# Kernel optimization log

Hardware: AMD Instinct MI355X
Metric: run time of the kernel (lower is better)

The kernel has to match this reference:

```python
import jax, jax.numpy as jnp
import numpy as np


def _sobel_filters():
    # 3D Sobel kernels for x, y, z directions, shape (3, 1, 3, 3, 3) in OIDHW.
    x = np.array([[[-1, 0, 1], [-2, 0, 2], [-1, 0, 1]],
                  [[-2, 0, 2], [-4, 0, 4], [-2, 0, 2]],
                  [[-1, 0, 1], [-2, 0, 2], [-1, 0, 1]]], dtype=np.float32)
    y = np.array([[[1, 2, 1], [0, 0, 0], [-1, -2, -1]],
                  [[2, 4, 2], [0, 0, 0], [-2, -4, -2]],
                  [[1, 2, 1], [0, 0, 0], [-1, -2, -1]]], dtype=np.float32)
    z = np.array([[[1, 2, 1], [2, 4, 2], [1, 2, 1]],
                  [[0, 0, 0], [0, 0, 0], [0, 0, 0]],
                  [[-1, -2, -1], [-2, -4, -2], [-1, -2, -1]]], dtype=np.float32)
    return jnp.asarray(np.stack([x, y, z])[:, None])  # (3,1,3,3,3)


_FILTERS = _sobel_filters()
_EPS = 1e-10


def gradient3d(x):
    # x: [B,1,D,H,W] -> gradient magnitude [B,1,D,H,W].
    # Single conv with 3 output channels == three separate torch conv3d + concat.
    g = jax.lax.conv_general_dilated(
        x, _FILTERS, window_strides=(1, 1, 1),
        padding=[(1, 1), (1, 1), (1, 1)],
        dimension_numbers=('NCDHW', 'OIDHW', 'NCDHW'))  # [B,3,D,H,W]
    return jnp.sqrt(jnp.sum(g * g, axis=1, keepdims=True) + _EPS)


def setup_inputs() -> dict:
    key = jax.random.key(0)
    k1, k2, k3 = jax.random.split(key, 3)
    shape = (2, 1, 192, 192, 192)
    pred = jax.random.normal(k1, shape, dtype=jnp.float32)
    gt_dose = jax.random.normal(k2, shape, dtype=jnp.float32)
    body_mask = (jax.random.uniform(k3, shape) > 0.3).astype(jnp.float32)
    return {"pred": pred, "gt_dose": gt_dose, "body_mask": body_mask}


def reference(pred, gt_dose, body_mask):
    mse = jnp.square(pred - gt_dose) * body_mask
    mge = jnp.square(gradient3d(gt_dose) - gradient3d(pred)) * body_mask
    return jnp.mean(mse + jnp.tanh(mge) * mse)
```

## Files before the change

### kernel.cpp

```cpp
#include <hip/hip_runtime.h>
#include <math.h>

#define W 192
#define H 192
#define DEPTH 192
#define BATCH 2
#define TW 64
#define TH 8
#define DC 12
#define HW (H * W)
#define VOL ((size_t)DEPTH * HW)
#define LROW 72
#define LPLANE (LROW * 10)
#define NPAIR ((DC + 2) / 2)
#define NITEM 720

__global__ __launch_bounds__(256) void sobel_loss_part(
    const float* __restrict__ pred, const float* __restrict__ gt,
    const float* __restrict__ mask, float* __restrict__ partials)
{
    __shared__ __align__(16) float lds[2 * 2 * LPLANE];

    const int tid = threadIdx.x;
    const int tx = blockIdx.x % 3;
    const int ty = blockIdx.x / 3;
    const int w0 = tx * TW, h0 = ty * TH;
    const int d0 = blockIdx.y * DC;
    const size_t base = (size_t)blockIdx.z * VOL;

    const int wy  = tid >> 5;
    const int wxo = (tid & 31) << 1;
    const size_t moff = base + (size_t)(h0 + wy) * W + (w0 + wxo);

    int it_ok[3], it_st[3], it_q[3], it_lds[3];
    size_t it_goff[3];
    const float* it_src[3];
    #pragma unroll
    for (int k = 0; k < 3; ++k) {
        int j = tid + 256 * k;
        int jj = (j < NITEM) ? j : 0;
        int a = jj / 360; int pj = jj - a * 360;
        int q = pj / 180; int e = pj - q * 180;
        int r = e / 18;   int c = e - r * 18;
        int y  = h0 - 1 + r;
        int xf = w0 - 4 + 4 * c;
        it_st[k]  = (j < NITEM);
        it_ok[k]  = it_st[k] && ((unsigned)y < (unsigned)H) && ((unsigned)xf < (unsigned)W);
        it_goff[k] = it_ok[k] ? ((size_t)y * W + xf) : 0;
        it_lds[k]  = ((a * 2 + q) * 10 + r) * LROW + 4 * c;
        it_q[k]    = q;
        it_src[k]  = a ? gt : pred;
    }

    float4 R[3];
    auto load_pair = [&](int s) {
        const int p0 = d0 - 1 + 2 * s;
        #pragma unroll
        for (int k = 0; k < 3; ++k) {
            const int p = p0 + it_q[k];
            const bool v = it_ok[k] && (p >= 0) && (p < DEPTH);
            R[k] = v ? *(const float4*)(it_src[k] + base + (size_t)p * HW + it_goff[k])
                     : make_float4(0.f, 0.f, 0.f, 0.f);
        }
    };

    float2 Mn = make_float2(0.f, 0.f), Mn1 = make_float2(0.f, 0.f);
    float2 Mc, Mc1;
    auto load_mask = [&](int s) {
        Mn  = *(const float2*)(mask + moff + (size_t)(d0 + 2 * s - 2) * HW);
        Mn1 = *(const float2*)(mask + moff + (size_t)(d0 + 2 * s - 1) * HW);
    };

    float dx[2][2][3], dy[2][2][3], sm[2][2][3], ct[2][2][2];
    #pragma unroll
    for (int a = 0; a < 2; ++a)
        #pragma unroll
        for (int o = 0; o < 2; ++o) {
            dx[a][o][0]=dx[a][o][1]=dx[a][o][2]=0.f;
            dy[a][o][0]=dy[a][o][1]=dy[a][o][2]=0.f;
            sm[a][o][0]=sm[a][o][1]=sm[a][o][2]=0.f;
            ct[a][o][0]=ct[a][o][1]=0.f;
        }
    float acc = 0.f;

    load_pair(0);

    for (int s = 0; s < NPAIR; ++s) {
        __syncthreads();
        #pragma unroll
        for (int k = 0; k < 3; ++k)
            if (it_st[k]) *(float4*)(lds + it_lds[k]) = R[k];
        __syncthreads();

        Mc = Mn; Mc1 = Mn1;
        if (s + 1 < NPAIR) {
            load_pair(s + 1);
            load_mask(s + 1);
        }

        #pragma unroll
        for (int q = 0; q < 2; ++q) {
            const int p = d0 - 1 + 2 * s + q;
            float e[2][3][4];
            #pragma unroll
            for (int a = 0; a < 2; ++a)
                #pragma unroll
                for (int r = 0; r < 3; ++r)
                    #pragma unroll
                    for (int c = 0; c < 4; ++c)
                        e[a][r][c] = lds[(a * 2 + q) * LPLANE + (wy + r) * LROW + wxo + 3 + c];

            #pragma unroll
            for (int a = 0; a < 2; ++a)
                #pragma unroll
                for (int o = 0; o < 2; ++o) {
                    float s0 = e[a][0][o] + 2.f * e[a][0][o+1] + e[a][0][o+2];
                    float s1 = e[a][1][o] + 2.f * e[a][1][o+1] + e[a][1][o+2];
                    float s2 = e[a][2][o] + 2.f * e[a][2][o+1] + e[a][2][o+2];
                    float dd0 = e[a][0][o+2] - e[a][0][o];
                    float dd1 = e[a][1][o+2] - e[a][1][o];
                    float dd2 = e[a][2][o+2] - e[a][2][o];
                    dx[a][o][0] = dx[a][o][1]; dx[a][o][1] = dx[a][o][2]; dx[a][o][2] = dd0 + 2.f * dd1 + dd2;
                    sm[a][o][0] = sm[a][o][1]; sm[a][o][1] = sm[a][o][2]; sm[a][o][2] = s0 + 2.f * s1 + s2;
                    dy[a][o][0] = dy[a][o][1]; dy[a][o][1] = dy[a][o][2]; dy[a][o][2] = s0 - s2;
                    ct[a][o][0] = ct[a][o][1]; ct[a][o][1] = e[a][1][o+1];
                }

            if (p >= d0 + 1) {
                const float2 M = q ? Mc1 : Mc;
                #pragma unroll
                for (int o = 0; o < 2; ++o) {
                    float gxa = dx[0][o][0] + 2.f * dx[0][o][1] + dx[0][o][2];
                    float gya = dy[0][o][0] + 2.f * dy[0][o][1] + dy[0][o][2];
                    float gza = sm[0][o][0] - sm[0][o][2];
                    float gxb = dx[1][o][0] + 2.f * dx[1][o][1] + dx[1][o][2];
                    float gyb = dy[1][o][0] + 2.f * dy[1][o][1] + dy[1][o][2];
                    float gzb = sm[1][o][0] - sm[1][o][2];
                    float ga = __builtin_amdgcn_sqrtf(gxa * gxa + gya * gya + gza * gza + 1e-10f);
                    float gb = __builtin_amdgcn_sqrtf(gxb * gxb + gyb * gyb + gzb * gzb + 1e-10f);
                    float m  = o ? M.y : M.x;
                    float dm = ct[0][o][0] - ct[1][o][0];
                    float mse = dm * dm * m;
                    float dg  = gb - ga;
                    float mge = dg * dg * m;
                    float ex = __expf(2.f * mge);
                    float t  = 1.f - 2.f * __builtin_amdgcn_rcpf(ex + 1.f);
                    acc += mse * (1.f + t);
                }
            }
        }
    }

    float v = acc;
    #pragma unroll
    for (int o = 32; o > 0; o >>= 1) v += __shfl_down(v, o, 64);
    __shared__ float red[4];
    if ((tid & 63) == 0) red[tid >> 6] = v;
    __syncthreads();
    if (tid == 0) {
        partials[(size_t)blockIdx.z * (gridDim.x * gridDim.y)
                 + (size_t)blockIdx.y * gridDim.x + blockIdx.x]
            = red[0] + red[1] + red[2] + red[3];
    }
}

__global__ __launch_bounds__(256) void reduce_final(
    const float* __restrict__ partials, int n, float* __restrict__ out)
{
    int tid = threadIdx.x;
    double s = 0.0;
    for (int i = tid; i < n; i += 256) s += (double)partials[i];
    #pragma unroll
    for (int o = 32; o > 0; o >>= 1) s += __shfl_down(s, o, 64);
    __shared__ double red[4];
    if ((tid & 63) == 0) red[tid >> 6] = s;
    __syncthreads();
    if (tid == 0) {
        double t = red[0] + red[1] + red[2] + red[3];
        const double ntot = (double)BATCH * (double)DEPTH * (double)H * (double)W;
        out[0] = (float)(t / ntot);
    }
}

extern "C" void kernel_launch(void* const* d_in, const int* in_sizes, int n_in,
                              void* d_out, int out_size, void* d_ws, size_t ws_size,
                              hipStream_t stream) {
    const float* pred = (const float*)d_in[0];
    const float* gt   = (const float*)d_in[1];
    const float* mask = (const float*)d_in[2];
    float* partials = (float*)d_ws;

    dim3 grid((W / TW) * (H / TH), DEPTH / DC, BATCH);
    sobel_loss_part<<<grid, 256, 0, stream>>>(pred, gt, mask, partials);

    int nparts = grid.x * grid.y * grid.z;
    reduce_final<<<1, 256, 0, stream>>>(partials, nparts, (float*)d_out);
}
```

Baseline: 185.3 us.

## Fuse final reduction via last-block atomic and double-buffer LDS planes

Replaces the separate reduction kernel with a last-block-done pattern: each block writes its partial, bumps an atomic counter, and the final block sums all partials. The LDS staging is double-buffered so one __syncthreads per depth step can be dropped. The depth chunk per block grows and a minimum occupancy hint is added, which cuts halo re-reads and block count but reduces parallelism. A memset launch is added to reset the counter each call.

```diff
diff --git a/kernel.cpp b/kernel.cpp
--- a/kernel.cpp
+++ b/kernel.cpp
@@ -7,19 +7,25 @@
 #define BATCH 2
 #define TW 64
 #define TH 8
-#define DC 12
+#define DC 16
 #define HW (H * W)
 #define VOL ((size_t)DEPTH * HW)
 #define LROW 72
 #define LPLANE (LROW * 10)
+#define LBUF (2 * 2 * LPLANE)
 #define NPAIR ((DC + 2) / 2)
 #define NITEM 720
-
-__global__ __launch_bounds__(256) void sobel_loss_part(
+#define GX ((W / TW) * (H / TH))
+#define GY (DEPTH / DC)
+#define NBLK (GX * GY * BATCH)
+#define COUNTER_OFF 7168
+
+__global__ __launch_bounds__(256, 7) void sobel_loss_fused(
     const float* __restrict__ pred, const float* __restrict__ gt,
-    const float* __restrict__ mask, float* __restrict__ partials)
+    const float* __restrict__ mask, float* __restrict__ partials,
+    unsigned int* __restrict__ counter, float* __restrict__ out)
 {
-    __shared__ __align__(16) float lds[2 * 2 * LPLANE];
+    __shared__ __align__(16) float lds[2][LBUF];
 
     const int tid = threadIdx.x;
     const int tx = blockIdx.x % 3;
@@ -86,10 +92,10 @@
     load_pair(0);
 
     for (int s = 0; s < NPAIR; ++s) {
-        __syncthreads();
+        float* buf = lds[s & 1];
         #pragma unroll
         for (int k = 0; k < 3; ++k)
-            if (it_st[k]) *(float4*)(lds + it_lds[k]) = R[k];
+            if (it_st[k]) *(float4*)(buf + it_lds[k]) = R[k];
         __syncthreads();
 
         Mc = Mn; Mc1 = Mn1;
@@ -108,7 +114,7 @@
                 for (int r = 0; r < 3; ++r)
                     #pragma unroll
                     for (int c = 0; c < 4; ++c)
-                        e[a][r][c] = lds[(a * 2 + q) * LPLANE + (wy + r) * LROW + wxo + 3 + c];
+                        e[a][r][c] = buf[(a * 2 + q) * LPLANE + (wy + r) * LROW + wxo + 3 + c];
 
             #pragma unroll
             for (int a = 0; a < 2; ++a)
@@ -154,31 +160,37 @@
     float v = acc;
     #pragma unroll
     for (int o = 32; o > 0; o >>= 1) v += __shfl_down(v, o, 64);
-    __shared__ float red[4];
-    if ((tid & 63) == 0) red[tid >> 6] = v;
+    float* redf = &lds[1][0];
+    if ((tid & 63) == 0) redf[tid >> 6] = v;
     __syncthreads();
+
+    unsigned int* lastp = (unsigned int*)&lds[0][0];
     if (tid == 0) {
-        partials[(size_t)blockIdx.z * (gridDim.x * gridDim.y)
-                 + (size_t)blockIdx.y * gridDim.x + blockIdx.x]
-            = red[0] + red[1] + red[2] + red[3];
-    }
-}
-
-__global__ __launch_bounds__(256) void reduce_final(
-    const float* __restrict__ partials, int n, float* __restrict__ out)
-{
-    int tid = threadIdx.x;
-    double s = 0.0;
-    for (int i = tid; i < n; i += 256) s += (double)partials[i];
-    #pragma unroll
-    for (int o = 32; o > 0; o >>= 1) s += __shfl_down(s, o, 64);
-    __shared__ double red[4];
-    if ((tid & 63) == 0) red[tid >> 6] = s;
+        float bs = redf[0] + redf[1] + redf[2] + redf[3];
+        int idx = blockIdx.z * (GX * GY) + blockIdx.y * GX + blockIdx.x;
+        partials[idx] = bs;
+        __threadfence();
+        unsigned int old = atomicAdd(counter, 1u);
+        *lastp = (old == (unsigned int)(NBLK - 1)) ? 1u : 0u;
+    }
     __syncthreads();
-    if (tid == 0) {
-        double t = red[0] + red[1] + red[2] + red[3];
-        const double ntot = (double)BATCH * (double)DEPTH * (double)H * (double)W;
-        out[0] = (float)(t / ntot);
+
+    if (*lastp) {
+        __threadfence();
+        double sd = 0.0;
+        for (int i = tid; i < NBLK; i += 256)
+            sd += (double)__hip_atomic_load(&partials[i], __ATOMIC_RELAXED,
+                                            __HIP_MEMORY_SCOPE_AGENT);
+        #pragma unroll
+        for (int o = 32; o > 0; o >>= 1) sd += __shfl_down(sd, o, 64);
+        double* dred = (double*)&lds[0][2];
+        if ((tid & 63) == 0) dred[tid >> 6] = sd;
+        __syncthreads();
+        if (tid == 0) {
+            double t = dred[0] + dred[1] + dred[2] + dred[3];
+            const double ntot = (double)BATCH * (double)DEPTH * (double)H * (double)W;
+            out[0] = (float)(t / ntot);
+        }
     }
 }
 
@@ -189,10 +201,10 @@
     const float* gt   = (const float*)d_in[1];
     const float* mask = (const float*)d_in[2];
     float* partials = (float*)d_ws;
-
-    dim3 grid((W / TW) * (H / TH), DEPTH / DC, BATCH);
-    sobel_loss_part<<<grid, 256, 0, stream>>>(pred, gt, mask, partials);
-
-    int nparts = grid.x * grid.y * grid.z;
-    reduce_final<<<1, 256, 0, stream>>>(partials, nparts, (float*)d_out);
+    unsigned int* counter = (unsigned int*)((char*)d_ws + COUNTER_OFF);
+
+    hipMemsetAsync(counter, 0, sizeof(unsigned int), stream);
+
+    dim3 grid(GX, GY, BATCH);
+    sobel_loss_fused<<<grid, 256, 0, stream>>>(pred, gt, mask, partials, counter, (float*)d_out);
 }
```

Measured after the change: 364.3 us. 96.6% more time.
